# Kernel optimization log

Measured on AMD Instinct MI355X. Metric: run time of the kernel, lower is better.

The kernel has to match this reference:

```python
import jax, jax.numpy as jnp
import numpy as np

N_NODES = 50000


def gcn_conv(x, src, dst, W, b):
    """PyG GCNConv: add self-loops, symmetric norm, linear, scatter-add, bias."""
    n = x.shape[0]
    loop = jnp.arange(n)
    s = jnp.concatenate([src, loop])  # sources incl. self-loops
    d = jnp.concatenate([dst, loop])  # targets incl. self-loops
    deg = jax.ops.segment_sum(jnp.ones(d.shape[0], dtype=x.dtype), d, num_segments=n)
    dinv = jnp.where(deg > 0, jax.lax.rsqrt(deg), 0.0).astype(x.dtype)
    norm = dinv[s] * dinv[d]                      # [E+N]
    h = x @ W                                      # [N, C_out]
    msg = h[s] * norm[:, None]                     # [E+N, C_out] gather + scale
    out = jax.ops.segment_sum(msg, d, num_segments=n)  # scatter-add to targets
    return out + b


def setup_inputs() -> dict:
    key = jax.random.key(0)
    k1, k2, k3, k4, k5 = jax.random.split(key, 5)
    in_c, hid_c, out_c = 128, 64, 64
    x = jax.random.normal(k1, (N_NODES, in_c), dtype=jnp.float32)
    edge_index = jax.random.randint(k2, (2, 1600000), 0, N_NODES, dtype=jnp.int64)
    # Glorot-style init for weights, zero bias (PyG defaults)
    W1 = jax.random.normal(k3, (in_c, hid_c), dtype=jnp.float32) * (1.0 / np.sqrt(in_c))
    b1 = jnp.zeros((hid_c,), dtype=jnp.float32)
    W2 = jax.random.normal(k4, (hid_c, out_c), dtype=jnp.float32) * (1.0 / np.sqrt(hid_c))
    b2 = jnp.zeros((out_c,), dtype=jnp.float32)
    return {"x": x, "edge_index": edge_index, "W1": W1, "b1": b1, "W2": W2, "b2": b2}


def reference(x, edge_index, W1, b1, W2, b2):
    src, dst = edge_index[0], edge_index[1]
    h = jax.nn.relu(gcn_conv(x, src, dst, W1, b1))
    z = gcn_conv(h, src, dst, W2, b2)
    return z
```

## Files before the change

### kernel.cpp

```cpp
#include <hip/hip_runtime.h>
#include <hip/hip_fp16.h>


#define NPB_SHIFT 7
#define NPB 128
#define NBMAX 1024
#define EPB 4096
#define KPB (EPB / 256)
#define EMAX 8192
#define CAP 4608
#define CSRSTRIDE 6656

typedef _Float16 f16x8 __attribute__((ext_vector_type(8)));
typedef float f32x4 __attribute__((ext_vector_type(4)));
union F16x8 { f16x8 v; __half2 h[4]; uint4 u; };

__global__ __launch_bounds__(256) void zero_kernel(int* __restrict__ p, int m,
                                                   int* __restrict__ zrow) {
    int i = blockIdx.x * 256 + threadIdx.x;
    if (i < m) p[i] = 0;
    if (blockIdx.x == 0 && threadIdx.x < 32) zrow[threadIdx.x] = 0;
}

__global__ __launch_bounds__(256) void bin_scatter_kernel(const int* __restrict__ src,
                                                          const int* __restrict__ dst, int E, int NB,
                                                          int* __restrict__ bucketCur,
                                                          int* __restrict__ pairs) {
    __shared__ int cntA[NBMAX];
    __shared__ int baseB[NBMAX];
    for (int i = threadIdx.x; i < NB; i += 256) cntA[i] = 0;
    __syncthreads();
    int base = blockIdx.x * EPB;
    int pk_[KPB], b_[KPB];
    #pragma unroll
    for (int k = 0; k < KPB; ++k) {
        int i = base + k * 256 + threadIdx.x;
        if (i < E) {
            int s = src[i], d = dst[i];
            pk_[k] = (s << NPB_SHIFT) | (d & (NPB - 1));
            b_[k] = d >> NPB_SHIFT;
            atomicAdd(&cntA[b_[k]], 1);
        } else {
            b_[k] = -1;
        }
    }
    __syncthreads();
    for (int i = threadIdx.x; i < NB; i += 256) {
        int c = cntA[i];
        baseB[i] = c ? atomicAdd(&bucketCur[i], c) : 0;
        cntA[i] = 0;
    }
    __syncthreads();
    #pragma unroll
    for (int k = 0; k < KPB; ++k) {
        if (b_[k] >= 0) {
            int off = atomicAdd(&cntA[b_[k]], 1);
            pairs[b_[k] * CAP + baseB[b_[k]] + off] = pk_[k];
        }
    }
}

__global__ __launch_bounds__(256) void build_csr_kernel(const int* __restrict__ pairs,
                                                        const int* __restrict__ bucketCnt,
                                                        int NB, int n,
                                                        int2* __restrict__ rowinfo,
                                                        float* __restrict__ dinv,
                                                        int* __restrict__ csr) {
    __shared__ int deg[NPB];
    __shared__ int cur[NPB];
    __shared__ int rowL[NPB];
    __shared__ int lcsr[EMAX];
    __shared__ int s_mP;
    int b = blockIdx.x;
    int nodeBase = b << NPB_SHIFT;
    int nNodes = min(NPB, n - nodeBase);
    int eBeg = b * CAP;
    int m = min(bucketCnt[b], CAP);
    int eEnd = eBeg + m;
    int Pb = b * CSRSTRIDE;
    for (int i = threadIdx.x; i < NPB; i += 256) { deg[i] = 0; cur[i] = 0; }
    __syncthreads();
    for (int e = eBeg + threadIdx.x; e < eEnd; e += 256)
        atomicAdd(&deg[pairs[e] & (NPB - 1)], 1);
    __syncthreads();
    if (threadIdx.x < 64) {
        int j0 = threadIdx.x * 2, j1 = j0 + 1;
        int p0 = (deg[j0] + 15) & ~15, p1 = (deg[j1] + 15) & ~15;
        int s = p0 + p1;
        int x = s;
        #pragma unroll
        for (int off = 1; off < 64; off <<= 1) {
            int y = __shfl_up(x, off);
            if ((int)threadIdx.x >= off) x += y;
        }
        int excl = x - s;
        rowL[j0] = excl;
        rowL[j1] = excl + p0;
        if (threadIdx.x == 63) s_mP = x;
    }
    __syncthreads();
    int mP = s_mP;
    for (int j = threadIdx.x; j < nNodes; j += 256) {
        rowinfo[nodeBase + j] = make_int2(Pb + rowL[j], (deg[j] + 15) & ~15);
        dinv[nodeBase + j] = 1.0f / sqrtf((float)(deg[j] + 1));
    }
    const int padEnt = n << NPB_SHIFT;
    if (mP <= EMAX) {
        for (int i = threadIdx.x; i < mP; i += 256) lcsr[i] = padEnt;
        __syncthreads();
        for (int e = eBeg + threadIdx.x; e < eEnd; e += 256) {
            int pk = pairs[e];
            int d = pk & (NPB - 1);
            int off = atomicAdd(&cur[d], 1);
            lcsr[rowL[d] + off] = pk & ~(NPB - 1);
        }
        __syncthreads();
        for (int i = threadIdx.x; i < mP; i += 256) csr[Pb + i] = lcsr[i];
    } else {
        for (int i = threadIdx.x; i < mP; i += 256) csr[Pb + i] = padEnt;
        __syncthreads();
        for (int e = eBeg + threadIdx.x; e < eEnd; e += 256) {
            int pk = pairs[e];
            int d = pk & (NPB - 1);
            int off = atomicAdd(&cur[d], 1);
            csr[Pb + rowL[d] + off] = pk & ~(NPB - 1);
        }
    }
}

template <int K, typename TIN>
__global__ __launch_bounds__(256, 2) void gemm_scale_kernel(const TIN* __restrict__ X,
                                                            const float* __restrict__ W,
                                                            const float* __restrict__ dinv,
                                                            __half* __restrict__ out, int n) {
    __shared__ _Float16 Wt[64][K + 8];
    for (int idx = threadIdx.x; idx < K * 64; idx += 256) {
        int k = idx >> 6, c = idx & 63;
        Wt[c][k] = (_Float16)W[idx];
    }
    __syncthreads();

    const int lane = threadIdx.x & 63;
    const int wid  = threadIdx.x >> 6;
    const int l15  = lane & 15;
    const int lg   = lane >> 4;
    const int r0 = (blockIdx.x * 4 + wid) * 16;
    if (r0 >= n) return;

    F16x8 bfr[K / 32][4];
    #pragma unroll
    for (int kt = 0; kt < K / 32; ++kt)
        #pragma unroll
        for (int ct = 0; ct < 4; ++ct)
            bfr[kt][ct].u = *reinterpret_cast<const uint4*>(&Wt[ct * 16 + l15][kt * 32 + lg * 8]);

    f32x4 acc[4] = {{0.f, 0.f, 0.f, 0.f}, {0.f, 0.f, 0.f, 0.f},
                    {0.f, 0.f, 0.f, 0.f}, {0.f, 0.f, 0.f, 0.f}};
    const int arow = min(r0 + l15, n - 1);
    #pragma unroll
    for (int kt = 0; kt < K / 32; ++kt) {
        F16x8 a;
        if constexpr (sizeof(TIN) == 4) {
            const float4* xp = reinterpret_cast<const float4*>(
                (const float*)X + (size_t)arow * K + kt * 32 + lg * 8);
            float4 v0 = xp[0], v1 = xp[1];
            a.h[0] = __float22half2_rn(make_float2(v0.x, v0.y));
            a.h[1] = __float22half2_rn(make_float2(v0.z, v0.w));
            a.h[2] = __float22half2_rn(make_float2(v1.x, v1.y));
            a.h[3] = __float22half2_rn(make_float2(v1.z, v1.w));
        } else {
            a.u = *reinterpret_cast<const uint4*>(
                (const __half*)X + (size_t)arow * K + kt * 32 + lg * 8);
        }
        #pragma unroll
        for (int ct = 0; ct < 4; ++ct)
            acc[ct] = __builtin_amdgcn_mfma_f32_16x16x32_f16(a.v, bfr[kt][ct].v, acc[ct], 0, 0, 0);
    }

    float dv[4];
    #pragma unroll
    for (int i = 0; i < 4; ++i) dv[i] = dinv[min(r0 + lg * 4 + i, n - 1)];
    #pragma unroll
    for (int ct = 0; ct < 4; ++ct) {
        #pragma unroll
        for (int i = 0; i < 4; ++i) {
            int row = r0 + lg * 4 + i;
            if (row < n)
                out[(size_t)row * 64 + ct * 16 + l15] = __float2half_rn(acc[ct][i] * dv[i]);
        }
    }
}

template <bool RELU, typename TOUT>
__global__ __launch_bounds__(256) void aggregate_kernel(const __half* __restrict__ hs,
                                                        const int2* __restrict__ rowinfo,
                                                        const int* __restrict__ csr,
                                                        const float* __restrict__ dinv,
                                                        const float* __restrict__ bias,
                                                        TOUT* __restrict__ out, int n) {
    const int lane = threadIdx.x & 63;
    const int half = lane >> 5;
    const int l32  = lane & 31;
    const int wid  = threadIdx.x >> 6;
    int node = blockIdx.x * 4 + wid;
    if (node >= n) return;

    const char* hsb = (const char*)hs + l32 * 4;
    int2 info = rowinfo[node];
    const int* base = csr + info.x;
    const int cnt = info.y;
    float a0 = 0.f, a1 = 0.f;
    for (int i = 16 * half; i < cnt; i += 32) {
        int4 c0 = *reinterpret_cast<const int4*>(base + i);
        int4 c1 = *reinterpret_cast<const int4*>(base + i + 4);
        int4 c2 = *reinterpret_cast<const int4*>(base + i + 8);
        int4 c3 = *reinterpret_cast<const int4*>(base + i + 12);
        float2 f0 = __half22float2(*(const __half2*)(hsb + c0.x));
        float2 f1 = __half22float2(*(const __half2*)(hsb + c0.y));
        float2 f2 = __half22float2(*(const __half2*)(hsb + c0.z));
        float2 f3 = __half22float2(*(const __half2*)(hsb + c0.w));
        float2 f4 = __half22float2(*(const __half2*)(hsb + c1.x));
        float2 f5 = __half22float2(*(const __half2*)(hsb + c1.y));
        float2 f6 = __half22float2(*(const __half2*)(hsb + c1.z));
        float2 f7 = __half22float2(*(const __half2*)(hsb + c1.w));
        float2 f8 = __half22float2(*(const __half2*)(hsb + c2.x));
        float2 f9 = __half22float2(*(const __half2*)(hsb + c2.y));
        float2 fa = __half22float2(*(const __half2*)(hsb + c2.z));
        float2 fb = __half22float2(*(const __half2*)(hsb + c2.w));
        float2 fc = __half22float2(*(const __half2*)(hsb + c3.x));
        float2 fd = __half22float2(*(const __half2*)(hsb + c3.y));
        float2 fe = __half22float2(*(const __half2*)(hsb + c3.z));
        float2 ff = __half22float2(*(const __half2*)(hsb + c3.w));
        a0 += (((f0.x + f1.x) + (f2.x + f3.x)) + ((f4.x + f5.x) + (f6.x + f7.x)))
            + (((f8.x + f9.x) + (fa.x + fb.x)) + ((fc.x + fd.x) + (fe.x + ff.x)));
        a1 += (((f0.y + f1.y) + (f2.y + f3.y)) + ((f4.y + f5.y) + (f6.y + f7.y)))
            + (((f8.y + f9.y) + (fa.y + fb.y)) + ((fc.y + fd.y) + (fe.y + ff.y)));
    }
    a0 += __shfl_xor(a0, 32);
    a1 += __shfl_xor(a1, 32);
    float2 fs = __half22float2(
        *(const __half2*)((const char*)hs + ((size_t)node << 7) + l32 * 4));
    a0 += fs.x;
    a1 += fs.y;

    if (half == 0) {
        float dv = dinv[node];
        float b0 = bias[2 * l32], b1 = bias[2 * l32 + 1];
        float r0 = fmaf(a0, dv, b0);
        float r1 = fmaf(a1, dv, b1);
        if (RELU) { r0 = fmaxf(r0, 0.f); r1 = fmaxf(r1, 0.f); }
        if constexpr (sizeof(TOUT) == 2) {
            *reinterpret_cast<__half2*>((__half*)out + (size_t)node * 64 + 2 * l32) =
                __float22half2_rn(make_float2(r0, r1));
        } else {
            *reinterpret_cast<float2*>((float*)out + (size_t)node * 64 + 2 * l32) =
                make_float2(r0, r1);
        }
    }
}

extern "C" void kernel_launch(void* const* d_in, const int* in_sizes, int n_in,
                              void* d_out, int out_size, void* d_ws, size_t ws_size,
                              hipStream_t stream) {
    const float* x  = (const float*)d_in[0];
    const int*   ei = (const int*)d_in[1];
    const float* W1 = (const float*)d_in[2];
    const float* b1 = (const float*)d_in[3];
    const float* W2 = (const float*)d_in[4];
    const float* b2 = (const float*)d_in[5];
    float* out = (float*)d_out;

    const int E = in_sizes[1] / 2;
    const int n = out_size / 64;
    const int NB = (n + NPB - 1) >> NPB_SHIFT;

    char* wsp = (char*)d_ws;
    auto carve = [&](size_t bytes) {
        char* p = wsp;
        wsp += (bytes + 255) & ~(size_t)255;
        return p;
    };
    float*  dinv      = (float*)carve((size_t)n * 4);
    int2*   rowinfo   = (int2*) carve((size_t)n * 8);
    int*    bucketCur = (int*)  carve((size_t)NBMAX * 4);
    int*    csr       = (int*)  carve((size_t)NB * CSRSTRIDE * 4);
    size_t  pairBytes = ((size_t)NB + 1) * CAP * 4;
    size_t  featF16   = (size_t)n * 64 * 2;
    size_t  bigBytes  = pairBytes > featF16 ? pairBytes : featF16;
    char*   big       = (char*)carve(bigBytes);
    int*    pairs     = (int*)big;
    __half* hbuf      = (__half*)big;
    __half* hsbuf     = (__half*)carve((size_t)(n + 1) * 64 * 2);

    const int* srcIdx = ei;
    const int* dstIdx = ei + E;
    const int scatterBlocks = (E + EPB - 1) / EPB;
    const int gemmBlocks = (n + 63) / 64;
    const int aggBlocks = (n + 3) / 4;

    zero_kernel<<<(NBMAX + 255) / 256, 256, 0, stream>>>(bucketCur, NBMAX,
                                                         (int*)(hsbuf + (size_t)n * 64));
    bin_scatter_kernel<<<scatterBlocks, 256, 0, stream>>>(srcIdx, dstIdx, E, NB, bucketCur, pairs);
    build_csr_kernel<<<NB, 256, 0, stream>>>(pairs, bucketCur, NB, n, rowinfo, dinv, csr);

    gemm_scale_kernel<128, float><<<gemmBlocks, 256, 0, stream>>>(x, W1, dinv, hsbuf, n);
    aggregate_kernel<true, __half><<<aggBlocks, 256, 0, stream>>>(hsbuf, rowinfo, csr, dinv,
                                                                  b1, hbuf, n);

    gemm_scale_kernel<64, __half><<<gemmBlocks, 256, 0, stream>>>(hbuf, W2, dinv, hsbuf, n);
    aggregate_kernel<false, float><<<aggBlocks, 256, 0, stream>>>(hsbuf, rowinfo, csr, dinv,
                                                                  b2, out, n);
}
```

Baseline: 115.3 us.

## Split aggregation channels into two 64-byte halves across separate blocks

Each node's 64 fp16 channels are now split into two 32-channel halves, handled by different blocks. Inside a wave, four 16-lane groups each walk a different slice of the neighbor list, which doubles the edge-level parallelism per wave. Block indices are arranged so that both channel halves of a tile of 16 nodes are processed by neighboring blocks. This is meant to raise memory-level parallelism for the random gathers and shorten per-node serial loops. The cost is that every block reads the CSR index list twice, uses half-size 64-byte gather segments, and needs an extra shuffle reduction.

After: 139.4 us. 20.8% more time.

```diff
diff --git a/kernel.cpp b/kernel.cpp
--- a/kernel.cpp
+++ b/kernel.cpp
@@ -199,61 +199,66 @@
                                                         const float* __restrict__ bias,
                                                         TOUT* __restrict__ out, int n) {
     const int lane = threadIdx.x & 63;
-    const int half = lane >> 5;
-    const int l32  = lane & 31;
+    const int qq   = lane >> 4;
+    const int cl   = lane & 15;
     const int wid  = threadIdx.x >> 6;
-    int node = blockIdx.x * 4 + wid;
+    const int t  = blockIdx.x >> 3;
+    const int q8 = blockIdx.x & 7;
+    const int cg  = q8 >> 2;
+    const int sub = q8 & 3;
+    int node = t * 16 + sub * 4 + wid;
     if (node >= n) return;
 
-    const char* hsb = (const char*)hs + l32 * 4;
+    const char* tl = (const char*)hs + cg * 64 + cl * 4;
     int2 info = rowinfo[node];
     const int* base = csr + info.x;
     const int cnt = info.y;
     float a0 = 0.f, a1 = 0.f;
-    for (int i = 16 * half; i < cnt; i += 32) {
+    for (int i = 16 * qq; i < cnt; i += 64) {
         int4 c0 = *reinterpret_cast<const int4*>(base + i);
         int4 c1 = *reinterpret_cast<const int4*>(base + i + 4);
         int4 c2 = *reinterpret_cast<const int4*>(base + i + 8);
         int4 c3 = *reinterpret_cast<const int4*>(base + i + 12);
-        float2 f0 = __half22float2(*(const __half2*)(hsb + c0.x));
-        float2 f1 = __half22float2(*(const __half2*)(hsb + c0.y));
-        float2 f2 = __half22float2(*(const __half2*)(hsb + c0.z));
-        float2 f3 = __half22float2(*(const __half2*)(hsb + c0.w));
-        float2 f4 = __half22float2(*(const __half2*)(hsb + c1.x));
-        float2 f5 = __half22float2(*(const __half2*)(hsb + c1.y));
-        float2 f6 = __half22float2(*(const __half2*)(hsb + c1.z));
-        float2 f7 = __half22float2(*(const __half2*)(hsb + c1.w));
-        float2 f8 = __half22float2(*(const __half2*)(hsb + c2.x));
-        float2 f9 = __half22float2(*(const __half2*)(hsb + c2.y));
-        float2 fa = __half22float2(*(const __half2*)(hsb + c2.z));
-        float2 fb = __half22float2(*(const __half2*)(hsb + c2.w));
-        float2 fc = __half22float2(*(const __half2*)(hsb + c3.x));
-        float2 fd = __half22float2(*(const __half2*)(hsb + c3.y));
-        float2 fe = __half22float2(*(const __half2*)(hsb + c3.z));
-        float2 ff = __half22float2(*(const __half2*)(hsb + c3.w));
+        float2 f0 = __half22float2(*(const __half2*)(tl + c0.x));
+        float2 f1 = __half22float2(*(const __half2*)(tl + c0.y));
+        float2 f2 = __half22float2(*(const __half2*)(tl + c0.z));
+        float2 f3 = __half22float2(*(const __half2*)(tl + c0.w));
+        float2 f4 = __half22float2(*(const __half2*)(tl + c1.x));
+        float2 f5 = __half22float2(*(const __half2*)(tl + c1.y));
+        float2 f6 = __half22float2(*(const __half2*)(tl + c1.z));
+        float2 f7 = __half22float2(*(const __half2*)(tl + c1.w));
+        float2 f8 = __half22float2(*(const __half2*)(tl + c2.x));
+        float2 f9 = __half22float2(*(const __half2*)(tl + c2.y));
+        float2 fa = __half22float2(*(const __half2*)(tl + c2.z));
+        float2 fb = __half22float2(*(const __half2*)(tl + c2.w));
+        float2 fc = __half22float2(*(const __half2*)(tl + c3.x));
+        float2 fd = __half22float2(*(const __half2*)(tl + c3.y));
+        float2 fe = __half22float2(*(const __half2*)(tl + c3.z));
+        float2 ff = __half22float2(*(const __half2*)(tl + c3.w));
         a0 += (((f0.x + f1.x) + (f2.x + f3.x)) + ((f4.x + f5.x) + (f6.x + f7.x)))
             + (((f8.x + f9.x) + (fa.x + fb.x)) + ((fc.x + fd.x) + (fe.x + ff.x)));
         a1 += (((f0.y + f1.y) + (f2.y + f3.y)) + ((f4.y + f5.y) + (f6.y + f7.y)))
             + (((f8.y + f9.y) + (fa.y + fb.y)) + ((fc.y + fd.y) + (fe.y + ff.y)));
     }
+    a0 += __shfl_xor(a0, 16);
+    a1 += __shfl_xor(a1, 16);
     a0 += __shfl_xor(a0, 32);
     a1 += __shfl_xor(a1, 32);
-    float2 fs = __half22float2(
-        *(const __half2*)((const char*)hs + ((size_t)node << 7) + l32 * 4));
+    float2 fs = __half22float2(*(const __half2*)(tl + ((size_t)node << 7)));
     a0 += fs.x;
     a1 += fs.y;
 
-    if (half == 0) {
+    if (lane < 16) {
         float dv = dinv[node];
-        float b0 = bias[2 * l32], b1 = bias[2 * l32 + 1];
+        float b0 = bias[cg * 32 + 2 * cl], b1 = bias[cg * 32 + 2 * cl + 1];
         float r0 = fmaf(a0, dv, b0);
         float r1 = fmaf(a1, dv, b1);
         if (RELU) { r0 = fmaxf(r0, 0.f); r1 = fmaxf(r1, 0.f); }
         if constexpr (sizeof(TOUT) == 2) {
-            *reinterpret_cast<__half2*>((__half*)out + (size_t)node * 64 + 2 * l32) =
+            *reinterpret_cast<__half2*>((__half*)out + (size_t)node * 64 + cg * 32 + 2 * cl) =
                 __float22half2_rn(make_float2(r0, r1));
         } else {
-            *reinterpret_cast<float2*>((float*)out + (size_t)node * 64 + 2 * l32) =
+            *reinterpret_cast<float2*>((float*)out + (size_t)node * 64 + cg * 32 + 2 * cl) =
                 make_float2(r0, r1);
         }
     }
@@ -296,7 +301,7 @@
     const int* dstIdx = ei + E;
     const int scatterBlocks = (E + EPB - 1) / EPB;
     const int gemmBlocks = (n + 63) / 64;
-    const int aggBlocks = (n + 3) / 4;
+    const int aggBlocks = 8 * ((n + 15) / 16);
 
     zero_kernel<<<(NBMAX + 255) / 256, 256, 0, stream>>>(bucketCur, NBMAX,
                                                          (int*)(hsbuf + (size_t)n * 64));
```
